# Performance work log

Measured on AMD Instinct MI355X. Metric: run time of the kernel, lower is better.

The kernel has to match this reference:

```python
import jax, jax.numpy as jnp
import numpy as np

N_NODES = 100000
N_EDGES = 1_000_000
NODE_DIM = 64
EDGE_DIM = 32
HIDDEN = 64


def _unif(key, shape, fan_in):
    bound = 1.0 / np.sqrt(fan_in)
    return jax.random.uniform(key, shape, jnp.float32, -bound, bound)


def setup_inputs() -> dict:
    key = jax.random.key(0)
    ks = jax.random.split(key, 11)
    node_features = jax.random.normal(ks[0], (N_NODES, NODE_DIM), jnp.float32)
    edge_index = jax.random.randint(ks[1], (2, N_EDGES), 0, N_NODES, dtype=jnp.int64)
    edge_features = jax.random.normal(ks[2], (N_EDGES, EDGE_DIM), jnp.float32)
    in_dim = 2 * NODE_DIM + EDGE_DIM
    # message MLP: Linear(in_dim, HIDDEN) -> ReLU -> Linear(HIDDEN, HIDDEN)
    W1 = _unif(ks[3], (HIDDEN, in_dim), in_dim)
    b1 = _unif(ks[4], (HIDDEN,), in_dim)
    W2 = _unif(ks[5], (HIDDEN, HIDDEN), HIDDEN)
    b2 = _unif(ks[6], (HIDDEN,), HIDDEN)
    # GRUCell(input=HIDDEN, hidden=NODE_DIM); gates stacked [r; z; n]
    w_ih = _unif(ks[7], (3 * NODE_DIM, HIDDEN), NODE_DIM)
    w_hh = _unif(ks[8], (3 * NODE_DIM, NODE_DIM), NODE_DIM)
    b_ih = _unif(ks[9], (3 * NODE_DIM,), NODE_DIM)
    b_hh = _unif(ks[10], (3 * NODE_DIM,), NODE_DIM)
    return {
        "node_features": node_features,
        "edge_index": edge_index,
        "edge_features": edge_features,
        "W1": W1, "b1": b1, "W2": W2, "b2": b2,
        "w_ih": w_ih, "w_hh": w_hh, "b_ih": b_ih, "b_hh": b_hh,
    }


def reference(node_features, edge_index, edge_features, W1, b1, W2, b2, w_ih, w_hh, b_ih, b_hh):
    src, dst = edge_index[0], edge_index[1]
    # gather endpoints and build message MLP input: [E, 2*node_dim+edge_dim]
    x = jnp.concatenate([node_features[src], node_features[dst], edge_features], axis=-1)
    h = jax.nn.relu(x @ W1.T + b1)
    messages = h @ W2.T + b2  # [E, HIDDEN]
    # scatter-add into per-node aggregates
    agg = jax.ops.segment_sum(messages, dst, num_segments=node_features.shape[0])
    # GRUCell(agg, node_features) with torch gate order [r, z, n]
    gi = agg @ w_ih.T + b_ih
    gh = node_features @ w_hh.T + b_hh
    i_r, i_z, i_n = jnp.split(gi, 3, axis=-1)
    h_r, h_z, h_n = jnp.split(gh, 3, axis=-1)
    r = jax.nn.sigmoid(i_r + h_r)
    z = jax.nn.sigmoid(i_z + h_z)
    n = jnp.tanh(i_n + r * h_n)
    return (1.0 - z) * n + z * node_features
```

## Files before the change

### kernel.cpp

```cpp
#include <hip/hip_runtime.h>
#include <hip/hip_bf16.h>

#define N_NODES 100000
#define N_EDGES 1000000
#define SCAN_CHUNK 1024
#define N_SCAN_BLKS ((N_NODES + SCAN_CHUNK - 1) / SCAN_CHUNK)

typedef __bf16 bf16x8 __attribute__((ext_vector_type(8)));
typedef float  f32x4  __attribute__((ext_vector_type(4)));

#define MFMA(a, b, c) __builtin_amdgcn_mfma_f32_16x16x32_bf16((a), (b), (c), 0, 0, 0)

__device__ __forceinline__ float sigmoid_f(float x) { return 1.f / (1.f + __expf(-x)); }
__device__ __forceinline__ float tanh_f(float x) {
    float cx = fminf(fmaxf(x, -30.f), 30.f);
    float e = __expf(-2.f * cx);
    return (1.f - e) / (1.f + e);
}

__global__ __launch_bounds__(256) void pq_kernel(
    const float* __restrict__ nf, const float* __restrict__ W1,
    const float* __restrict__ b1,
    __bf16* __restrict__ Pb, __bf16* __restrict__ Qb)
{
    const int lane = threadIdx.x & 63;
    const int r = lane & 15, g = lane >> 4;

    bf16x8 Bs[4][2], Bd[4][2];
    #pragma unroll
    for (int nt = 0; nt < 4; ++nt)
        #pragma unroll
        for (int kk = 0; kk < 2; ++kk) {
            const float* ws = &W1[(nt * 16 + r) * 160 + kk * 32 + g * 8];
            const float* wd = ws + 64;
            f32x4 s0 = *(const f32x4*)ws, s1 = *(const f32x4*)(ws + 4);
            f32x4 d0 = *(const f32x4*)wd, d1 = *(const f32x4*)(wd + 4);
            #pragma unroll
            for (int j = 0; j < 4; ++j) {
                Bs[nt][kk][j] = (__bf16)s0[j]; Bs[nt][kk][j + 4] = (__bf16)s1[j];
                Bd[nt][kk][j] = (__bf16)d0[j]; Bd[nt][kk][j + 4] = (__bf16)d1[j];
            }
        }
    float b1v[4];
    #pragma unroll
    for (int nt = 0; nt < 4; ++nt) b1v[nt] = b1[nt * 16 + r];

    const int wid = blockIdx.x * (blockDim.x >> 6) + (threadIdx.x >> 6);
    const int nW  = gridDim.x * (blockDim.x >> 6);
    for (int t = wid; t < N_NODES / 16; t += nW) {
        const int base = t * 16;
        bf16x8 A[2];
        #pragma unroll
        for (int kk = 0; kk < 2; ++kk) {
            const float* p = &nf[(size_t)(base + r) * 64 + kk * 32 + g * 8];
            f32x4 v0 = *(const f32x4*)p, v1 = *(const f32x4*)(p + 4);
            #pragma unroll
            for (int j = 0; j < 4; ++j) { A[kk][j] = (__bf16)v0[j]; A[kk][j + 4] = (__bf16)v1[j]; }
        }
        f32x4 accP[4] = {}, accQ[4] = {};
        #pragma unroll
        for (int nt = 0; nt < 4; ++nt)
            #pragma unroll
            for (int kk = 0; kk < 2; ++kk) {
                accP[nt] = MFMA(A[kk], Bs[nt][kk], accP[nt]);
                accQ[nt] = MFMA(A[kk], Bd[nt][kk], accQ[nt]);
            }
        #pragma unroll
        for (int nt = 0; nt < 4; ++nt)
            #pragma unroll
            for (int rr = 0; rr < 4; ++rr) {
                const int node = base + g * 4 + rr;
                const int col  = nt * 16 + r;
                Pb[(size_t)node * 64 + col] = (__bf16)(accP[nt][rr] + b1v[nt]);
                Qb[(size_t)node * 64 + col] = (__bf16)accQ[nt][rr];
            }
    }
}

__global__ __launch_bounds__(256) void hist_kernel(
    const int* __restrict__ ei, int* __restrict__ cnt)
{
    const int* dstI = ei + N_EDGES;
    for (int e = blockIdx.x * blockDim.x + threadIdx.x; e < N_EDGES;
         e += gridDim.x * blockDim.x)
        atomicAdd(&cnt[dstI[e]], 1);
}

__global__ __launch_bounds__(256) void scanA_kernel(
    const int* __restrict__ cnt, int* __restrict__ blkSum)
{
    const int lane = threadIdx.x & 63, w = threadIdx.x >> 6;
    int base = blockIdx.x * SCAN_CHUNK + threadIdx.x * 4;
    int s = 0;
    #pragma unroll
    for (int j = 0; j < 4; ++j) if (base + j < N_NODES) s += cnt[base + j];
    #pragma unroll
    for (int o = 32; o > 0; o >>= 1) s += __shfl_down(s, o);
    __shared__ int wt[4];
    if (lane == 0) wt[w] = s;
    __syncthreads();
    if (threadIdx.x == 0) blkSum[blockIdx.x] = wt[0] + wt[1] + wt[2] + wt[3];
}

__global__ void scanB_kernel(int* __restrict__ blkSum)
{
    const int lane = threadIdx.x;
    int carry = 0;
    for (int c = 0; c < N_SCAN_BLKS; c += 64) {
        int v = (c + lane < N_SCAN_BLKS) ? blkSum[c + lane] : 0;
        int inc = v;
        #pragma unroll
        for (int o = 1; o < 64; o <<= 1) {
            int t = __shfl_up(inc, o);
            if (lane >= o) inc += t;
        }
        int ex = inc - v;
        if (c + lane < N_SCAN_BLKS) blkSum[c + lane] = carry + ex;
        carry += __shfl(inc, 63);
    }
}

__global__ __launch_bounds__(256) void scanC_kernel(
    const int* __restrict__ cnt, const int* __restrict__ blkSum,
    int* __restrict__ off, int* __restrict__ cur)
{
    const int lane = threadIdx.x & 63, w = threadIdx.x >> 6;
    int base = blockIdx.x * SCAN_CHUNK + threadIdx.x * 4;
    int v[4];
    int tsum = 0;
    #pragma unroll
    for (int j = 0; j < 4; ++j) {
        v[j] = (base + j < N_NODES) ? cnt[base + j] : 0;
        tsum += v[j];
    }
    int inc = tsum;
    #pragma unroll
    for (int o = 1; o < 64; o <<= 1) {
        int t = __shfl_up(inc, o);
        if (lane >= o) inc += t;
    }
    __shared__ int wt[4];
    if (lane == 63) wt[w] = inc;
    __syncthreads();
    int woff = 0;
    for (int k = 0; k < w; ++k) woff += wt[k];
    int running = blkSum[blockIdx.x] + woff + inc - tsum;
    #pragma unroll
    for (int j = 0; j < 4; ++j) {
        if (base + j < N_NODES) {
            off[base + j] = running;
            cur[base + j] = running;
            if (base + j == N_NODES - 1) off[N_NODES] = running + v[j];
            running += v[j];
        }
    }
}

__global__ __launch_bounds__(256) void scatter_kernel(
    const int* __restrict__ ei, int* __restrict__ cur,
    int* __restrict__ slotSrc, int* __restrict__ posA)
{
    const int* srcI = ei;
    const int* dstI = ei + N_EDGES;
    for (int e = blockIdx.x * blockDim.x + threadIdx.x; e < N_EDGES;
         e += gridDim.x * blockDim.x) {
        int p = atomicAdd(&cur[dstI[e]], 1);
        slotSrc[p] = srcI[e];
        posA[e] = p;
    }
}

__global__ __launch_bounds__(256) void e_kernel(
    const float* __restrict__ ef, const float* __restrict__ W1,
    const int* __restrict__ posA, __bf16* __restrict__ Eb)
{
    const int lane = threadIdx.x & 63;
    const int r = lane & 15, g = lane >> 4;

    bf16x8 Be[4];
    #pragma unroll
    for (int nt = 0; nt < 4; ++nt) {
        const float* w = &W1[(nt * 16 + r) * 160 + 128 + g * 8];
        f32x4 w0 = *(const f32x4*)w, w1 = *(const f32x4*)(w + 4);
        #pragma unroll
        for (int j = 0; j < 4; ++j) { Be[nt][j] = (__bf16)w0[j]; Be[nt][j + 4] = (__bf16)w1[j]; }
    }

    const int wid = blockIdx.x * (blockDim.x >> 6) + (threadIdx.x >> 6);
    const int nW  = gridDim.x * (blockDim.x >> 6);
    for (int t = wid; t < N_EDGES / 16; t += nW) {
        const int base = t * 16;
        bf16x8 Ae;
        {
            const float* p = &ef[(size_t)(base + r) * 32 + g * 8];
            f32x4 v0 = *(const f32x4*)p, v1 = *(const f32x4*)(p + 4);
            #pragma unroll
            for (int j = 0; j < 4; ++j) { Ae[j] = (__bf16)v0[j]; Ae[j + 4] = (__bf16)v1[j]; }
        }
        f32x4 accT[4] = {};
        #pragma unroll
        for (int nt = 0; nt < 4; ++nt) accT[nt] = MFMA(Ae, Be[nt], accT[nt]);

        int4 p4 = *(const int4*)(posA + base + g * 4);
        const int* pp = (const int*)&p4;
        #pragma unroll
        for (int rr = 0; rr < 4; ++rr) {
            __bf16* row = Eb + (size_t)pp[rr] * 64;
            #pragma unroll
            for (int nt = 0; nt < 4; ++nt)
                row[nt * 16 + r] = (__bf16)accT[nt][rr];
        }
    }
}

__global__ __launch_bounds__(256) void gather_kernel(
    const int* __restrict__ off, const int* __restrict__ slotSrc,
    const __bf16* __restrict__ Eb, const __bf16* __restrict__ Pb,
    const __bf16* __restrict__ Qb, float* __restrict__ Hsum)
{
    const int lane = threadIdx.x & 63;
    const int wid = blockIdx.x * (blockDim.x >> 6) + (threadIdx.x >> 6);
    const int nW  = gridDim.x * (blockDim.x >> 6);
    for (int n = wid; n < N_NODES; n += nW) {
        const int o0 = off[n], o1 = off[n + 1];
        const int m = o1 - o0;
        float q = (float)Qb[(size_t)n * 64 + lane];
        float acc = 0.f;
        int sl = (lane < m) ? slotSrc[o0 + lane] : 0;
        int i = 0;
        for (; i + 8 <= m && i + 8 <= 64; i += 8) {
            float pv[8], evv[8];
            #pragma unroll
            for (int j = 0; j < 8; ++j) {
                int s = __shfl(sl, i + j);
                pv[j]  = (float)Pb[(size_t)s * 64 + lane];
                evv[j] = (float)Eb[(size_t)(o0 + i + j) * 64 + lane];
            }
            #pragma unroll
            for (int j = 0; j < 8; ++j)
                acc += fmaxf(pv[j] + evv[j] + q, 0.f);
        }
        for (; i < m; ++i) {
            int s = (i < 64) ? __shfl(sl, i) : slotSrc[o0 + i];
            float pv = (float)Pb[(size_t)s * 64 + lane];
            float ev = (float)Eb[(size_t)(o0 + i) * 64 + lane];
            acc += fmaxf(pv + ev + q, 0.f);
        }
        Hsum[(size_t)n * 64 + lane] = acc;
    }
}

__global__ __launch_bounds__(256) void prep_kernel(
    const float* __restrict__ w_ih, const float* __restrict__ W2,
    const float* __restrict__ b2, float* __restrict__ M, float* __restrict__ b2i)
{
    int tid = blockIdx.x * blockDim.x + threadIdx.x;
    if (tid < 192 * 64) {
        int d = tid >> 6, k = tid & 63;
        float s = 0.f;
        #pragma unroll 8
        for (int j = 0; j < 64; ++j) s += w_ih[d * 64 + j] * W2[j * 64 + k];
        M[tid] = s;
    }
    if (tid < 192) {
        float s = 0.f;
        for (int j = 0; j < 64; ++j) s += w_ih[tid * 64 + j] * b2[j];
        b2i[tid] = s;
    }
}

__global__ __launch_bounds__(256) void gru_kernel(
    const float* __restrict__ nf, const float* __restrict__ Hsum,
    const float* __restrict__ M, const float* __restrict__ w_hh,
    const float* __restrict__ b_ih, const float* __restrict__ b_hh,
    const float* __restrict__ b2i, const int* __restrict__ cnt,
    float* __restrict__ out)
{
    __shared__ __bf16 w_lds[2 * 192 * 64];
    for (int ch = threadIdx.x; ch < 3072; ch += 256) {
        int mat = ch >> 11;
        mat = ch / 1536;
        int rr  = (ch - mat * 1536) >> 3;
        int cc  = ch & 7;
        const float* sp = (mat == 0 ? M : w_hh) + rr * 64 + cc * 8;
        f32x4 a = *(const f32x4*)sp, b = *(const f32x4*)(sp + 4);
        bf16x8 v;
        #pragma unroll
        for (int j = 0; j < 4; ++j) { v[j] = (__bf16)a[j]; v[j + 4] = (__bf16)b[j]; }
        *(bf16x8*)&w_lds[((mat * 192 + rr) * 64) + ((cc ^ (rr & 7)) * 8)] = v;
    }
    __syncthreads();

    const int lane = threadIdx.x & 63;
    const int r = lane & 15, g = lane >> 4;
    const int wid = blockIdx.x * (blockDim.x >> 6) + (threadIdx.x >> 6);
    const int nW  = gridDim.x * (blockDim.x >> 6);

    float br[4], bz[4], bin_[4], bhn_[4], c2r[4], c2z[4], c2n[4];
    #pragma unroll
    for (int nt = 0; nt < 4; ++nt) {
        const int d = nt * 16 + r;
        br[nt]   = b_ih[d] + b_hh[d];
        bz[nt]   = b_ih[64 + d] + b_hh[64 + d];
        bin_[nt] = b_ih[128 + d];
        bhn_[nt] = b_hh[128 + d];
        c2r[nt] = b2i ? b2i[d] : 0.f;
        c2z[nt] = b2i ? b2i[64 + d] : 0.f;
        c2n[nt] = b2i ? b2i[128 + d] : 0.f;
    }
    const int swz = r & 7;

    for (int t = wid; t < N_NODES / 16; t += nW) {
        const int base = t * 16;
        bf16x8 aaH[2], aaL[2], ahH[2], ahL[2];
        #pragma unroll
        for (int kk = 0; kk < 2; ++kk) {
            const float* pa = &Hsum[(size_t)(base + r) * 64 + kk * 32 + g * 8];
            const float* ph = &nf  [(size_t)(base + r) * 64 + kk * 32 + g * 8];
            f32x4 a0 = *(const f32x4*)pa, a1 = *(const f32x4*)(pa + 4);
            f32x4 h0 = *(const f32x4*)ph, h1 = *(const f32x4*)(ph + 4);
            #pragma unroll
            for (int j = 0; j < 4; ++j) {
                float av0 = a0[j], av1 = a1[j], hv0 = h0[j], hv1 = h1[j];
                __bf16 x;
                x = (__bf16)av0; aaH[kk][j]     = x; aaL[kk][j]     = (__bf16)(av0 - (float)x);
                x = (__bf16)av1; aaH[kk][j + 4] = x; aaL[kk][j + 4] = (__bf16)(av1 - (float)x);
                x = (__bf16)hv0; ahH[kk][j]     = x; ahL[kk][j]     = (__bf16)(hv0 - (float)x);
                x = (__bf16)hv1; ahH[kk][j + 4] = x; ahL[kk][j + 4] = (__bf16)(hv1 - (float)x);
            }
        }

        f32x4 accR[4] = {}, accZ[4] = {}, accIN[4] = {}, accHN[4] = {};
        #pragma unroll
        for (int c = 0; c < 3; ++c)
            #pragma unroll
            for (int nt = 0; nt < 4; ++nt) {
                const int row = c * 64 + nt * 16 + r;
                f32x4 ai = {}, ah = {};
                #pragma unroll
                for (int kk = 0; kk < 2; ++kk) {
                    const int cc = (kk * 4 + g) ^ swz;
                    bf16x8 Bi = *(const bf16x8*)&w_lds[row * 64 + cc * 8];
                    bf16x8 Bh = *(const bf16x8*)&w_lds[(192 + row) * 64 + cc * 8];
                    ai = MFMA(aaH[kk], Bi, ai);
                    ai = MFMA(aaL[kk], Bi, ai);
                    ah = MFMA(ahH[kk], Bh, ah);
                    ah = MFMA(ahL[kk], Bh, ah);
                }
                if (c == 0)      accR[nt] = ai + ah;
                else if (c == 1) accZ[nt] = ai + ah;
                else             { accIN[nt] = ai; accHN[nt] = ah; }
            }
        #pragma unroll
        for (int nt = 0; nt < 4; ++nt)
            #pragma unroll
            for (int rr = 0; rr < 4; ++rr) {
                const int node = base + g * 4 + rr;
                const int d    = nt * 16 + r;
                float dg = cnt ? (float)cnt[node] : 0.f;
                float rg = sigmoid_f(accR[nt][rr] + br[nt] + dg * c2r[nt]);
                float zg = sigmoid_f(accZ[nt][rr] + bz[nt] + dg * c2z[nt]);
                float ng = tanh_f(accIN[nt][rr] + bin_[nt] + dg * c2n[nt] +
                                  rg * (accHN[nt][rr] + bhn_[nt]));
                float hv = nf[(size_t)node * 64 + d];
                out[(size_t)node * 64 + d] = (1.f - zg) * ng + zg * hv;
            }
    }
}

#define LDH 68
__global__ __launch_bounds__(256) void edge_kernel_fb(
    const int* __restrict__ ei, const float* __restrict__ ef,
    const float* __restrict__ W1, const float* __restrict__ W2,
    const float* __restrict__ b2,
    const __bf16* __restrict__ Pb, const __bf16* __restrict__ Qb,
    float* __restrict__ agg)
{
    __shared__ float lds_h[4][16 * LDH];
    const int lane = threadIdx.x & 63;
    const int r = lane & 15, g = lane >> 4;
    float* hb = lds_h[threadIdx.x >> 6];
    const int* srcI = ei;
    const int* dstI = ei + N_EDGES;

    bf16x8 Be[4];
    #pragma unroll
    for (int nt = 0; nt < 4; ++nt) {
        const float* w = &W1[(nt * 16 + r) * 160 + 128 + g * 8];
        f32x4 w0 = *(const f32x4*)w, w1 = *(const f32x4*)(w + 4);
        #pragma unroll
        for (int j = 0; j < 4; ++j) { Be[nt][j] = (__bf16)w0[j]; Be[nt][j + 4] = (__bf16)w1[j]; }
    }
    bf16x8 B2[4][2];
    #pragma unroll
    for (int nt = 0; nt < 4; ++nt)
        #pragma unroll
        for (int kk = 0; kk < 2; ++kk) {
            const float* w = &W2[(nt * 16 + r) * 64 + kk * 32 + g * 8];
            f32x4 w0 = *(const f32x4*)w, w1 = *(const f32x4*)(w + 4);
            #pragma unroll
            for (int j = 0; j < 4; ++j) { B2[nt][kk][j] = (__bf16)w0[j]; B2[nt][kk][j + 4] = (__bf16)w1[j]; }
        }
    float b2v[4];
    #pragma unroll
    for (int nt = 0; nt < 4; ++nt) b2v[nt] = b2[nt * 16 + r];

    const int wid = blockIdx.x * (blockDim.x >> 6) + (threadIdx.x >> 6);
    const int nW  = gridDim.x * (blockDim.x >> 6);
    for (int t = wid; t < N_EDGES / 16; t += nW) {
        const int base = t * 16;
        const int er = base + r;
        const int es = srcI[er], ed = dstI[er];
        bf16x8 Ae;
        {
            const float* p = &ef[(size_t)er * 32 + g * 8];
            f32x4 v0 = *(const f32x4*)p, v1 = *(const f32x4*)(p + 4);
            #pragma unroll
            for (int j = 0; j < 4; ++j) { Ae[j] = (__bf16)v0[j]; Ae[j + 4] = (__bf16)v1[j]; }
        }
        f32x4 accT[4] = {};
        #pragma unroll
        for (int nt = 0; nt < 4; ++nt) accT[nt] = MFMA(Ae, Be[nt], accT[nt]);
        #pragma unroll
        for (int nt = 0; nt < 4; ++nt)
            #pragma unroll
            for (int rr = 0; rr < 4; ++rr)
                hb[(g * 4 + rr) * LDH + nt * 16 + r] = accT[nt][rr];
        bf16x8 A2[2];
        #pragma unroll
        for (int kk = 0; kk < 2; ++kk) {
            const int k = kk * 32 + g * 8;
            const float* hp = &hb[r * LDH + k];
            f32x4 h0 = *(const f32x4*)hp, h1 = *(const f32x4*)(hp + 4);
            bf16x8 p8 = *(const bf16x8*)(Pb + (size_t)es * 64 + k);
            bf16x8 q8 = *(const bf16x8*)(Qb + (size_t)ed * 64 + k);
            #pragma unroll
            for (int j = 0; j < 4; ++j) {
                A2[kk][j]     = (__bf16)fmaxf(h0[j] + (float)p8[j]     + (float)q8[j],     0.f);
                A2[kk][j + 4] = (__bf16)fmaxf(h1[j] + (float)p8[j + 4] + (float)q8[j + 4], 0.f);
            }
        }
        f32x4 accM[4] = {};
        #pragma unroll
        for (int nt = 0; nt < 4; ++nt)
            #pragma unroll
            for (int kk = 0; kk < 2; ++kk)
                accM[nt] = MFMA(A2[kk], B2[nt][kk], accM[nt]);
        int4 d4 = *(const int4*)(dstI + base + g * 4);
        const int* dd = (const int*)&d4;
        #pragma unroll
        for (int rr = 0; rr < 4; ++rr) {
            float* dp = agg + (size_t)dd[rr] * 64;
            #pragma unroll
            for (int nt = 0; nt < 4; ++nt)
                atomicAdd(dp + nt * 16 + r, accM[nt][rr] + b2v[nt]);
        }
    }
}

extern "C" void kernel_launch(void* const* d_in, const int* in_sizes, int n_in,
                              void* d_out, int out_size, void* d_ws, size_t ws_size,
                              hipStream_t stream) {
    const float* nf  = (const float*)d_in[0];
    const int*   ei  = (const int*)  d_in[1];
    const float* ef  = (const float*)d_in[2];
    const float* W1  = (const float*)d_in[3];
    const float* b1  = (const float*)d_in[4];
    const float* W2  = (const float*)d_in[5];
    const float* b2  = (const float*)d_in[6];
    const float* wih = (const float*)d_in[7];
    const float* whh = (const float*)d_in[8];
    const float* bih = (const float*)d_in[9];
    const float* bhh = (const float*)d_in[10];
    float* out = (float*)d_out;

    char* ws = (char*)d_ws;
    size_t off_b = 0;
    auto alloc = [&](size_t bytes) { char* p = ws + off_b; off_b = (off_b + bytes + 255) & ~(size_t)255; return p; };
    int*    cnt     = (int*)   alloc((size_t)N_NODES * 4);
    int*    offA    = (int*)   alloc((size_t)(N_NODES + 1) * 4);
    int*    cur     = (int*)   alloc((size_t)N_NODES * 4);
    int*    blkSum  = (int*)   alloc((size_t)N_SCAN_BLKS * 4);
    int*    posA    = (int*)   alloc((size_t)N_EDGES * 4);
    int*    slotSrc = (int*)   alloc((size_t)N_EDGES * 4);
    __bf16* Eb      = (__bf16*)alloc((size_t)N_EDGES * 64 * 2);
    __bf16* Pb      = (__bf16*)alloc((size_t)N_NODES * 64 * 2);
    __bf16* Qb      = (__bf16*)alloc((size_t)N_NODES * 64 * 2);
    float*  Hsum    = (float*) alloc((size_t)N_NODES * 64 * 4);
    float*  M       = (float*) alloc((size_t)192 * 64 * 4);
    float*  b2i     = (float*) alloc((size_t)192 * 4);
    const size_t need = off_b;

    if (ws_size >= need) {
        hipMemsetAsync(cnt, 0, (size_t)N_NODES * 4, stream);
        hist_kernel   <<<1024, 256, 0, stream>>>(ei, cnt);
        scanA_kernel  <<<N_SCAN_BLKS, 256, 0, stream>>>(cnt, blkSum);
        scanB_kernel  <<<1, 64, 0, stream>>>(blkSum);
        scanC_kernel  <<<N_SCAN_BLKS, 256, 0, stream>>>(cnt, blkSum, offA, cur);
        pq_kernel     <<<1563, 256, 0, stream>>>(nf, W1, b1, Pb, Qb);
        prep_kernel   <<<48, 256, 0, stream>>>(wih, W2, b2, M, b2i);
        scatter_kernel<<<1024, 256, 0, stream>>>(ei, cur, slotSrc, posA);
        e_kernel      <<<2048, 256, 0, stream>>>(ef, W1, posA, Eb);
        gather_kernel <<<4096, 256, 0, stream>>>(offA, slotSrc, Eb, Pb, Qb, Hsum);
        gru_kernel    <<<1563, 256, 0, stream>>>(nf, Hsum, M, whh, bih, bhh, b2i, cnt, out);
    } else {
        float*  agg = (float*)ws;
        __bf16* Pf  = (__bf16*)(ws + (size_t)N_NODES * 64 * 4);
        __bf16* Qf  = (__bf16*)(ws + (size_t)N_NODES * 64 * 4 + (size_t)N_NODES * 64 * 2);
        hipMemsetAsync(agg, 0, (size_t)N_NODES * 64 * 4, stream);
        pq_kernel     <<<1563, 256, 0, stream>>>(nf, W1, b1, Pf, Qf);
        edge_kernel_fb<<<2048, 256, 0, stream>>>(ei, ef, W1, W2, b2, Pf, Qf, agg);
        gru_kernel    <<<1563, 256, 0, stream>>>(nf, agg, wih, whh, bih, bhh, nullptr, nullptr, out);
    }
}
```

Baseline: 575.6 us.

## Fuse edge-feature projection and CSR gather into one LDS-staged message kernel

Replaces the separate e_kernel (which wrote per-edge bf16 projections Eb to global memory in CSR order) and gather_kernel with a single msg_kernel. Each block takes a contiguous chunk of 256 CSR slots, computes the edge-feature projection with MFMA into shared memory, then reduces per destination node from LDS. Nodes that straddle chunk boundaries are combined with atomicAdd, which requires an extra memset of Hsum. The scatter now stores (src, edge id) pairs so the kernel can read edge features indirectly. This drops the 128 MB Eb round trip, at the cost of uncoalesced edge-feature reads and some atomics.

```diff
diff --git a/kernel.cpp b/kernel.cpp
--- a/kernel.cpp
+++ b/kernel.cpp
@@ -5,6 +5,8 @@
 #define N_EDGES 1000000
 #define SCAN_CHUNK 1024
 #define N_SCAN_BLKS ((N_NODES + SCAN_CHUNK - 1) / SCAN_CHUNK)
+#define NPB 256
+#define HST 68
 
 typedef __bf16 bf16x8 __attribute__((ext_vector_type(8)));
 typedef float  f32x4  __attribute__((ext_vector_type(4)));
@@ -158,95 +160,14 @@
 
 __global__ __launch_bounds__(256) void scatter_kernel(
     const int* __restrict__ ei, int* __restrict__ cur,
-    int* __restrict__ slotSrc, int* __restrict__ posA)
+    int2* __restrict__ slots)
 {
     const int* srcI = ei;
     const int* dstI = ei + N_EDGES;
     for (int e = blockIdx.x * blockDim.x + threadIdx.x; e < N_EDGES;
          e += gridDim.x * blockDim.x) {
         int p = atomicAdd(&cur[dstI[e]], 1);
-        slotSrc[p] = srcI[e];
-        posA[e] = p;
-    }
-}
-
-__global__ __launch_bounds__(256) void e_kernel(
-    const float* __restrict__ ef, const float* __restrict__ W1,
-    const int* __restrict__ posA, __bf16* __restrict__ Eb)
-{
-    const int lane = threadIdx.x & 63;
-    const int r = lane & 15, g = lane >> 4;
-
-    bf16x8 Be[4];
-    #pragma unroll
-    for (int nt = 0; nt < 4; ++nt) {
-        const float* w = &W1[(nt * 16 + r) * 160 + 128 + g * 8];
-        f32x4 w0 = *(const f32x4*)w, w1 = *(const f32x4*)(w + 4);
-        #pragma unroll
-        for (int j = 0; j < 4; ++j) { Be[nt][j] = (__bf16)w0[j]; Be[nt][j + 4] = (__bf16)w1[j]; }
-    }
-
-    const int wid = blockIdx.x * (blockDim.x >> 6) + (threadIdx.x >> 6);
-    const int nW  = gridDim.x * (blockDim.x >> 6);
-    for (int t = wid; t < N_EDGES / 16; t += nW) {
-        const int base = t * 16;
-        bf16x8 Ae;
-        {
-            const float* p = &ef[(size_t)(base + r) * 32 + g * 8];
-            f32x4 v0 = *(const f32x4*)p, v1 = *(const f32x4*)(p + 4);
-            #pragma unroll
-            for (int j = 0; j < 4; ++j) { Ae[j] = (__bf16)v0[j]; Ae[j + 4] = (__bf16)v1[j]; }
-        }
-        f32x4 accT[4] = {};
-        #pragma unroll
-        for (int nt = 0; nt < 4; ++nt) accT[nt] = MFMA(Ae, Be[nt], accT[nt]);
-
-        int4 p4 = *(const int4*)(posA + base + g * 4);
-        const int* pp = (const int*)&p4;
-        #pragma unroll
-        for (int rr = 0; rr < 4; ++rr) {
-            __bf16* row = Eb + (size_t)pp[rr] * 64;
-            #pragma unroll
-            for (int nt = 0; nt < 4; ++nt)
-                row[nt * 16 + r] = (__bf16)accT[nt][rr];
-        }
-    }
-}
-
-__global__ __launch_bounds__(256) void gather_kernel(
-    const int* __restrict__ off, const int* __restrict__ slotSrc,
-    const __bf16* __restrict__ Eb, const __bf16* __restrict__ Pb,
-    const __bf16* __restrict__ Qb, float* __restrict__ Hsum)
-{
-    const int lane = threadIdx.x & 63;
-    const int wid = blockIdx.x * (blockDim.x >> 6) + (threadIdx.x >> 6);
-    const int nW  = gridDim.x * (blockDim.x >> 6);
-    for (int n = wid; n < N_NODES; n += nW) {
-        const int o0 = off[n], o1 = off[n + 1];
-        const int m = o1 - o0;
-        float q = (float)Qb[(size_t)n * 64 + lane];
-        float acc = 0.f;
-        int sl = (lane < m) ? slotSrc[o0 + lane] : 0;
-        int i = 0;
-        for (; i + 8 <= m && i + 8 <= 64; i += 8) {
-            float pv[8], evv[8];
-            #pragma unroll
-            for (int j = 0; j < 8; ++j) {
-                int s = __shfl(sl, i + j);
-                pv[j]  = (float)Pb[(size_t)s * 64 + lane];
-                evv[j] = (float)Eb[(size_t)(o0 + i + j) * 64 + lane];
-            }
-            #pragma unroll
-            for (int j = 0; j < 8; ++j)
-                acc += fmaxf(pv[j] + evv[j] + q, 0.f);
-        }
-        for (; i < m; ++i) {
-            int s = (i < 64) ? __shfl(sl, i) : slotSrc[o0 + i];
-            float pv = (float)Pb[(size_t)s * 64 + lane];
-            float ev = (float)Eb[(size_t)(o0 + i) * 64 + lane];
-            acc += fmaxf(pv + ev + q, 0.f);
-        }
-        Hsum[(size_t)n * 64 + lane] = acc;
+        slots[p] = make_int2(srcI[e], e);
     }
 }
 
@@ -269,6 +190,89 @@
     }
 }
 
+__global__ __launch_bounds__(256) void msg_kernel(
+    const int* __restrict__ offA, const int2* __restrict__ slots,
+    const float* __restrict__ ef, const float* __restrict__ W1,
+    const __bf16* __restrict__ Pb, const __bf16* __restrict__ Qb,
+    float* __restrict__ Hsum)
+{
+    __shared__ float h[NPB * HST];
+    __shared__ int nlo_s;
+    const int p0 = blockIdx.x * NPB;
+    const int p1 = min(p0 + NPB, N_EDGES);
+    const int cntP = p1 - p0;
+    const int lane = threadIdx.x & 63;
+    const int w = threadIdx.x >> 6;
+    const int r = lane & 15, g = lane >> 4;
+
+    bf16x8 Be[4];
+    #pragma unroll
+    for (int nt = 0; nt < 4; ++nt) {
+        const float* wp = &W1[(nt * 16 + r) * 160 + 128 + g * 8];
+        f32x4 w0 = *(const f32x4*)wp, w1 = *(const f32x4*)(wp + 4);
+        #pragma unroll
+        for (int j = 0; j < 4; ++j) { Be[nt][j] = (__bf16)w0[j]; Be[nt][j + 4] = (__bf16)w1[j]; }
+    }
+
+    if (threadIdx.x == 0) {
+        int lo = 0, hi = N_NODES - 1;
+        while (lo < hi) { int mid = (lo + hi) >> 1; if (offA[mid + 1] > p0) hi = mid; else lo = mid + 1; }
+        nlo_s = lo;
+    }
+
+    const int ntile = cntP >> 4;
+    for (int t = w; t < ntile; t += 4) {
+        const int pb = p0 + t * 16;
+        int2 sl = slots[pb + r];
+        const float* ep = &ef[(size_t)sl.y * 32 + g * 8];
+        f32x4 v0 = *(const f32x4*)ep, v1 = *(const f32x4*)(ep + 4);
+        bf16x8 Ae;
+        #pragma unroll
+        for (int j = 0; j < 4; ++j) { Ae[j] = (__bf16)v0[j]; Ae[j + 4] = (__bf16)v1[j]; }
+        f32x4 accT[4] = {};
+        #pragma unroll
+        for (int nt = 0; nt < 4; ++nt) accT[nt] = MFMA(Ae, Be[nt], accT[nt]);
+        #pragma unroll
+        for (int nt = 0; nt < 4; ++nt)
+            #pragma unroll
+            for (int rr = 0; rr < 4; ++rr)
+                h[(t * 16 + g * 4 + rr) * HST + nt * 16 + r] = accT[nt][rr];
+    }
+    __syncthreads();
+
+    const int nlo = nlo_s;
+    for (int n = nlo + w; n < N_NODES; n += 4) {
+        const int on0 = offA[n], on1 = offA[n + 1];
+        if (on0 >= p1) break;
+        const int lo_ = max(on0, p0), hi_ = min(on1, p1);
+        const int m = hi_ - lo_;
+        if (m <= 0) continue;
+        const int lb = lo_ - p0;
+        float q = (float)Qb[(size_t)n * 64 + lane];
+        float acc = 0.f;
+        int sl = (lane < m) ? slots[lo_ + lane].x : 0;
+        int i = 0;
+        for (; i + 8 <= m && i + 8 <= 64; i += 8) {
+            float pv[8], hv[8];
+            #pragma unroll
+            for (int j = 0; j < 8; ++j) {
+                int s = __shfl(sl, i + j);
+                pv[j] = (float)Pb[(size_t)s * 64 + lane];
+                hv[j] = h[(lb + i + j) * HST + lane];
+            }
+            #pragma unroll
+            for (int j = 0; j < 8; ++j)
+                acc += fmaxf(hv[j] + pv[j] + q, 0.f);
+        }
+        for (; i < m; ++i) {
+            int s = (i < 64) ? __shfl(sl, i) : slots[lo_ + i].x;
+            acc += fmaxf(h[(lb + i) * HST + lane] + (float)Pb[(size_t)s * 64 + lane] + q, 0.f);
+        }
+        if (on0 >= p0 && on1 <= p1) Hsum[(size_t)n * 64 + lane] = acc;
+        else                        atomicAdd(&Hsum[(size_t)n * 64 + lane], acc);
+    }
+}
+
 __global__ __launch_bounds__(256) void gru_kernel(
     const float* __restrict__ nf, const float* __restrict__ Hsum,
     const float* __restrict__ M, const float* __restrict__ w_hh,
@@ -278,8 +282,7 @@
 {
     __shared__ __bf16 w_lds[2 * 192 * 64];
     for (int ch = threadIdx.x; ch < 3072; ch += 256) {
-        int mat = ch >> 11;
-        mat = ch / 1536;
+        int mat = ch / 1536;
         int rr  = (ch - mat * 1536) >> 3;
         int cc  = ch & 7;
         const float* sp = (mat == 0 ? M : w_hh) + rr * 64 + cc * 8;
@@ -386,8 +389,8 @@
     bf16x8 Be[4];
     #pragma unroll
     for (int nt = 0; nt < 4; ++nt) {
-        const float* w = &W1[(nt * 16 + r) * 160 + 128 + g * 8];
-        f32x4 w0 = *(const f32x4*)w, w1 = *(const f32x4*)(w + 4);
+        const float* wp = &W1[(nt * 16 + r) * 160 + 128 + g * 8];
+        f32x4 w0 = *(const f32x4*)wp, w1 = *(const f32x4*)(wp + 4);
         #pragma unroll
         for (int j = 0; j < 4; ++j) { Be[nt][j] = (__bf16)w0[j]; Be[nt][j + 4] = (__bf16)w1[j]; }
     }
@@ -396,8 +399,8 @@
     for (int nt = 0; nt < 4; ++nt)
         #pragma unroll
         for (int kk = 0; kk < 2; ++kk) {
-            const float* w = &W2[(nt * 16 + r) * 64 + kk * 32 + g * 8];
-            f32x4 w0 = *(const f32x4*)w, w1 = *(const f32x4*)(w + 4);
+            const float* wp = &W2[(nt * 16 + r) * 64 + kk * 32 + g * 8];
+            f32x4 w0 = *(const f32x4*)wp, w1 = *(const f32x4*)(wp + 4);
             #pragma unroll
             for (int j = 0; j < 4; ++j) { B2[nt][kk][j] = (__bf16)w0[j]; B2[nt][kk][j + 4] = (__bf16)w1[j]; }
         }
@@ -481,9 +484,7 @@
     int*    offA    = (int*)   alloc((size_t)(N_NODES + 1) * 4);
     int*    cur     = (int*)   alloc((size_t)N_NODES * 4);
     int*    blkSum  = (int*)   alloc((size_t)N_SCAN_BLKS * 4);
-    int*    posA    = (int*)   alloc((size_t)N_EDGES * 4);
-    int*    slotSrc = (int*)   alloc((size_t)N_EDGES * 4);
-    __bf16* Eb      = (__bf16*)alloc((size_t)N_EDGES * 64 * 2);
+    int2*   slots   = (int2*)  alloc((size_t)N_EDGES * 8);
     __bf16* Pb      = (__bf16*)alloc((size_t)N_NODES * 64 * 2);
     __bf16* Qb      = (__bf16*)alloc((size_t)N_NODES * 64 * 2);
     float*  Hsum    = (float*) alloc((size_t)N_NODES * 64 * 4);
@@ -493,15 +494,16 @@
 
     if (ws_size >= need) {
         hipMemsetAsync(cnt, 0, (size_t)N_NODES * 4, stream);
+        hipMemsetAsync(Hsum, 0, (size_t)N_NODES * 64 * 4, stream);
         hist_kernel   <<<1024, 256, 0, stream>>>(ei, cnt);
         scanA_kernel  <<<N_SCAN_BLKS, 256, 0, stream>>>(cnt, blkSum);
         scanB_kernel  <<<1, 64, 0, stream>>>(blkSum);
         scanC_kernel  <<<N_SCAN_BLKS, 256, 0, stream>>>(cnt, blkSum, offA, cur);
+        scatter_kernel<<<1024, 256, 0, stream>>>(ei, cur, slots);
         pq_kernel     <<<1563, 256, 0, stream>>>(nf, W1, b1, Pb, Qb);
         prep_kernel   <<<48, 256, 0, stream>>>(wih, W2, b2, M, b2i);
-        scatter_kernel<<<1024, 256, 0, stream>>>(ei, cur, slotSrc, posA);
-        e_kernel      <<<2048, 256, 0, stream>>>(ef, W1, posA, Eb);
-        gather_kernel <<<4096, 256, 0, stream>>>(offA, slotSrc, Eb, Pb, Qb, Hsum);
+        msg_kernel    <<<(N_EDGES + NPB - 1) / NPB, 256, 0, stream>>>(
+                          offA, slots, ef, W1, Pb, Qb, Hsum);
         gru_kernel    <<<1563, 256, 0, stream>>>(nf, Hsum, M, whh, bih, bhh, b2i, cnt, out);
     } else {
         float*  agg = (float*)ws;
```

Result: slower. 646.3 us (+12.3%).
